# Kernel tuning notes

Hardware: AMD Instinct MI355X
Metric: run time of the kernel (lower is better)

Reference implementation:

```python
import jax, jax.numpy as jnp
import numpy as np
import math

# static configuration
SPATIAL_SHAPES = [(100, 150), (50, 75), (25, 38), (13, 19)]  # (H, W) per level
EMBED, HEADS, LEVELS, POINTS = 256, 8, 4, 4
HEAD_DIM = EMBED // HEADS
BS = 2
NV = sum(h * w for h, w in SPATIAL_SHAPES)  # 19947
NQ = NV  # encoder-style self-attention (value = query)


def _offset_bias():
    # replicate torch _init_weights grid init for sampling_offsets bias
    thetas = np.arange(HEADS, dtype=np.float32) * (2.0 * math.pi / HEADS)
    grid = np.stack([np.cos(thetas), np.sin(thetas)], -1)  # [H,2]
    grid = grid / np.abs(grid).max(-1, keepdims=True)
    grid = np.tile(grid[:, None, None, :], (1, LEVELS, POINTS, 1))
    for i in range(POINTS):
        grid[:, :, i, :] *= (i + 1)
    return jnp.asarray(grid.reshape(-1), dtype=jnp.float32)


def setup_inputs() -> dict:
    key = jax.random.key(0)
    ks = jax.random.split(key, 8)
    sc = 1.0 / math.sqrt(EMBED)
    return {
        "query": jax.random.normal(ks[0], (BS, NQ, EMBED), jnp.float32),
        "reference_points": jax.random.uniform(ks[1], (BS, NQ, LEVELS, 2), jnp.float32),
        "spatial_shapes": jnp.asarray(SPATIAL_SHAPES, dtype=jnp.int32),
        "W_off": jax.random.normal(ks[2], (EMBED, HEADS * LEVELS * POINTS * 2), jnp.float32) * 0.01,
        "b_off": _offset_bias(),
        "W_attn": jax.random.normal(ks[3], (EMBED, HEADS * LEVELS * POINTS), jnp.float32) * 0.01,
        "b_attn": jnp.zeros((HEADS * LEVELS * POINTS,), jnp.float32),
        "W_val": jax.random.normal(ks[4], (EMBED, EMBED), jnp.float32) * sc,
        "b_val": jnp.zeros((EMBED,), jnp.float32),
        "W_out": jax.random.normal(ks[5], (EMBED, EMBED), jnp.float32) * sc,
        "b_out": jnp.zeros((EMBED,), jnp.float32),
    }


def _bilinear_sample(value_l, loc_l, H, W):
    # value_l: [bs, H*W, heads, hd]; loc_l: [bs, nq, heads, P, 2] normalized coords
    # grid_sample semantics: align_corners=False, padding_mode='zeros'
    x = loc_l[..., 0] * W - 0.5
    y = loc_l[..., 1] * H - 0.5
    x0 = jnp.floor(x)
    y0 = jnp.floor(y)
    dx = x - x0
    dy = y - y0
    x0i = x0.astype(jnp.int32)
    y0i = y0.astype(jnp.int32)

    def gather(xi, yi):
        valid = (xi >= 0) & (xi < W) & (yi >= 0) & (yi < H)  # [bs,nq,h,P]
        idx = jnp.clip(yi, 0, H - 1) * W + jnp.clip(xi, 0, W - 1)
        bs, nq, h, P = idx.shape
        idx2 = idx.transpose(0, 1, 3, 2).reshape(bs, nq * P, h)[..., None]
        v = jnp.take_along_axis(value_l, idx2, axis=1)  # [bs, nq*P, h, hd]
        v = v.reshape(bs, nq, P, h, -1).transpose(0, 1, 3, 2, 4)  # [bs,nq,h,P,hd]
        return v * valid[..., None]

    w00 = ((1 - dx) * (1 - dy))[..., None]
    w01 = (dx * (1 - dy))[..., None]
    w10 = ((1 - dx) * dy)[..., None]
    w11 = (dx * dy)[..., None]
    return (gather(x0i, y0i) * w00 + gather(x0i + 1, y0i) * w01
            + gather(x0i, y0i + 1) * w10 + gather(x0i + 1, y0i + 1) * w11)


def reference(query, reference_points, spatial_shapes, W_off, b_off, W_attn, b_attn,
              W_val, b_val, W_out, b_out):
    bs, nq, _ = query.shape
    # value = query (encoder self-attn), identity = query
    value = (query @ W_val + b_val).reshape(bs, NV, HEADS, HEAD_DIM)
    offs = (query @ W_off + b_off).reshape(bs, nq, HEADS, LEVELS, POINTS, 2)
    attw = jax.nn.softmax((query @ W_attn + b_attn).reshape(bs, nq, HEADS, LEVELS * POINTS), axis=-1)
    attw = attw.reshape(bs, nq, HEADS, LEVELS, POINTS)
    # offset normalizer: (W, H) per level
    norm = jnp.stack([spatial_shapes[:, 1], spatial_shapes[:, 0]], -1).astype(query.dtype)
    loc = reference_points[:, :, None, :, None, :] + offs / norm[None, None, None, :, None, :]

    out = jnp.zeros((bs, nq, HEADS, HEAD_DIM), query.dtype)
    start = 0
    for lvl, (H, W) in enumerate(SPATIAL_SHAPES):
        value_l = value[:, start:start + H * W]  # static slice
        start += H * W
        sampled = _bilinear_sample(value_l, loc[:, :, :, lvl], H, W)  # [bs,nq,h,P,hd]
        out = out + jnp.einsum('bnhpc,bnhp->bnhc', sampled, attw[:, :, :, lvl, :])

    out = out.reshape(bs, nq, EMBED) @ W_out + b_out
    return out + query  # dropout(p=0) + identity
```

## Files before the change

### kernel.cpp

```cpp
#include <hip/hip_runtime.h>
#include <math.h>

#define HEADS     8
#define LEVELS    4
#define POINTS    4
#define HEAD_DIM  32
#define EMBED     256
#define NQ        19947
#define NV        19947
#define BS        2
#define M_ROWS    (BS * NQ)

typedef _Float16 h8 __attribute__((ext_vector_type(8)));
typedef _Float16 h4 __attribute__((ext_vector_type(4)));
typedef _Float16 h2 __attribute__((ext_vector_type(2)));
typedef float    f32x4 __attribute__((ext_vector_type(4)));
typedef unsigned short ushort8 __attribute__((ext_vector_type(8)));

static __device__ __forceinline__ int lvl_H(int l) {
    constexpr int v[4] = {100, 50, 25, 13}; return v[l];
}
static __device__ __forceinline__ int lvl_W(int l) {
    constexpr int v[4] = {150, 75, 38, 19}; return v[l];
}
static __device__ __forceinline__ int lvl_start(int l) {
    constexpr int v[4] = {0, 15000, 18750, 19700}; return v[l];
}

static __device__ __forceinline__ unsigned short f2h(float f) {
    _Float16 h = (_Float16)f;
    return __builtin_bit_cast(unsigned short, h);
}

static __device__ __forceinline__ void gload_lds16(const void* g, void* l) {
    __builtin_amdgcn_global_load_lds(
        (const __attribute__((address_space(1))) void*)g,
        (__attribute__((address_space(3))) void*)l, 16, 0, 0);
}

static __device__ __forceinline__ void pkacc_u(h2* acc, uint4 u, unsigned wbits) {
    const h2 wv = __builtin_bit_cast(h2, wbits);
    acc[0] = __builtin_bit_cast(h2, u.x) * wv + acc[0];
    acc[1] = __builtin_bit_cast(h2, u.y) * wv + acc[1];
    acc[2] = __builtin_bit_cast(h2, u.z) * wv + acc[2];
    acc[3] = __builtin_bit_cast(h2, u.w) * wv + acc[3];
}

__global__ __launch_bounds__(256) void pack_weights_kernel(
    const float* __restrict__ Wv, const float* __restrict__ Wo,
    const float* __restrict__ Wa, const float* __restrict__ Wout,
    unsigned short* __restrict__ Wcat, unsigned short* __restrict__ WoutT)
{
    const int tid = blockIdx.x * 256 + threadIdx.x;
    if (tid >= 896 * 32) return;
    const int row = tid >> 5;
    const int k8  = tid & 31;
    const float* src; int n_local, N; unsigned short* dstb; int r_local;
    if (row < 256)      { src = Wv;   n_local = row;       N = 256; dstb = Wcat;  r_local = row; }
    else if (row < 512) { src = Wo;   n_local = row - 256; N = 256; dstb = Wcat;  r_local = row; }
    else if (row < 640) { src = Wa;   n_local = row - 512; N = 128; dstb = Wcat;  r_local = row; }
    else                { src = Wout; n_local = row - 640; N = 256; dstb = WoutT; r_local = row - 640; }
    const int k = k8 * 8;
    ushort8 o;
    #pragma unroll
    for (int j = 0; j < 8; ++j)
        o[j] = f2h(src[(size_t)(k + j) * N + n_local]);
    const int g  = k8 >> 3;
    const int u2 = (k8 & 7) ^ (r_local & 7);
    *(ushort8*)((char*)dstb + (size_t)r_local * 512 + g * 128 + u2 * 16) = o;
}

template <int EPI>
__global__ __launch_bounds__(256) void mfma_gemm_kernel(
    const float* __restrict__ Aq,
    const unsigned short* __restrict__ Ah,
    const unsigned short* __restrict__ Bh,
    unsigned short* __restrict__ value_h,
    unsigned short* __restrict__ oa,
    const float* __restrict__ b_val, const float* __restrict__ b_off,
    const float* __restrict__ b_attn,
    const float* __restrict__ b_out,
    const float* __restrict__ qres,
    float* __restrict__ out)
{
    __shared__ alignas(16) char As[16384];
    __shared__ alignas(16) char Bs[16384];

    constexpr int NB = (EPI == 0) ? 5 : 2;
    const int id  = blockIdx.x;
    const int grp = id / (8 * NB);
    const int rem = id - grp * (8 * NB);
    const int bx  = grp * 8 + (rem & 7);
    const int by  = rem >> 3;

    const int t    = threadIdx.x;
    const int wid  = t >> 6;
    const int lane = t & 63;
    const int l15  = lane & 15;
    const int lhi  = lane >> 4;
    const int wr   = wid >> 1;
    const int wc   = wid & 1;
    const int m0   = bx * 128;
    const int n0   = by * 128;

    f32x4 acc[4][4] = {};

    auto stage = [&](int ks) {
        #pragma unroll
        for (int j = 0; j < 4; ++j) {
            const int q  = j * 256 + wid * 64 + lane;
            const int tr = q >> 3;
            const int u  = q & 7;
            int gr = m0 + tr; gr = gr < M_ROWS ? gr : (M_ROWS - 1);
            if (EPI == 0) {
                const float* src = Aq + (size_t)gr * 256 + ks * 64 + u * 8;
                const float4 v0 = *(const float4*)(src);
                const float4 v1 = *(const float4*)(src + 4);
                ushort8 o;
                o[0] = f2h(v0.x); o[1] = f2h(v0.y);
                o[2] = f2h(v0.z); o[3] = f2h(v0.w);
                o[4] = f2h(v1.x); o[5] = f2h(v1.y);
                o[6] = f2h(v1.z); o[7] = f2h(v1.w);
                *(ushort8*)&As[tr * 128 + (unsigned)(u ^ (tr & 7)) * 16] = o;
            } else {
                gload_lds16((const char*)Ah + (size_t)gr * 512 + ks * 128 + u * 16,
                            As + (j * 256 + wid * 64) * 16);
            }
            const int gn = n0 + tr;
            gload_lds16((const char*)Bh + (size_t)gn * 512 + ks * 128 + u * 16,
                        Bs + (j * 256 + wid * 64) * 16);
        }
    };

    stage(0);
    for (int ks = 0; ks < 4; ++ks) {
        __syncthreads();
        #pragma unroll
        for (int kc = 0; kc < 2; ++kc) {
            h8 a[4], b[4];
            #pragma unroll
            for (int i = 0; i < 4; ++i) {
                const int tr = wr * 64 + i * 16 + l15;
                const int ua = (kc * 4 + lhi) ^ (tr & 7);
                a[i] = *(const h8*)&As[tr * 128 + ua * 16];
                const int tn = wc * 64 + i * 16 + l15;
                const int ub = (kc * 4 + lhi) ^ (tn & 7);
                b[i] = *(const h8*)&Bs[tn * 128 + ub * 16];
            }
            #pragma unroll
            for (int i = 0; i < 4; ++i)
                #pragma unroll
                for (int j2 = 0; j2 < 4; ++j2)
                    acc[i][j2] = __builtin_amdgcn_mfma_f32_16x16x32_f16(
                        a[i], b[j2], acc[i][j2], 0, 0, 0);
        }
        if (ks < 3) { __syncthreads(); stage(ks + 1); }
    }

    if (EPI == 0) {
        if (by < 2) {
            #pragma unroll
            for (int j2 = 0; j2 < 4; ++j2) {
                const int gn = n0 + wc * 64 + j2 * 16 + l15;
                const float bias = b_val[gn];
                const int h = gn >> 5, ch = gn & 31;
                #pragma unroll
                for (int i = 0; i < 4; ++i) {
                    #pragma unroll
                    for (int r = 0; r < 4; ++r) {
                        const int gm = m0 + wr * 64 + i * 16 + lhi * 4 + r;
                        if (gm >= M_ROWS) continue;
                        const int bb  = gm >= NQ;
                        const int pix = gm - bb * NQ;
                        value_h[(((size_t)bb * 8 + h) * NV + pix) * 32 + ch] =
                            f2h(acc[i][j2][r] + bias);
                    }
                }
            }
        } else {
            #pragma unroll
            for (int j2 = 0; j2 < 4; ++j2) {
                const int gn  = n0 + wc * 64 + j2 * 16 + l15;
                const int col = gn - 256;
                const float bias = (col < 256) ? b_off[col] : b_attn[col - 256];
                #pragma unroll
                for (int i = 0; i < 4; ++i) {
                    #pragma unroll
                    for (int r = 0; r < 4; ++r) {
                        const int gm = m0 + wr * 64 + i * 16 + lhi * 4 + r;
                        if (gm >= M_ROWS) continue;
                        oa[(size_t)gm * 384 + col] = f2h(acc[i][j2][r] + bias);
                    }
                }
            }
        }
    } else {
        #pragma unroll
        for (int j2 = 0; j2 < 4; ++j2) {
            const int gn = n0 + wc * 64 + j2 * 16 + l15;
            const float bias = b_out[gn];
            #pragma unroll
            for (int i = 0; i < 4; ++i) {
                #pragma unroll
                for (int r = 0; r < 4; ++r) {
                    const int gm = m0 + wr * 64 + i * 16 + lhi * 4 + r;
                    if (gm >= M_ROWS) continue;
                    out[(size_t)gm * 256 + gn] =
                        acc[i][j2][r] + bias + qres[(size_t)gm * 256 + gn];
                }
            }
        }
    }
}

__global__ __launch_bounds__(256) void sample_kernel_v13(
    const unsigned short* __restrict__ value,
    const _Float16* __restrict__ oa,
    const float* __restrict__ refp,
    unsigned short* __restrict__ outa_h)
{
    __shared__ uint4 sw_lds[16][34];

    const int bx    = blockIdx.x;
    const int h     = bx & 7;
    const int chunk = bx >> 3;
    const int g     = threadIdx.x >> 3;
    const int l8    = threadIdx.x & 7;
    const int row   = chunk * 32 + g;
    const bool valid = row < M_ROWS;

    if (valid && l8 < 4) {
        const int lvl = l8;
        const _Float16* oar = oa + (size_t)row * 384;
        const h8 oxy = *(const h8*)(oar + h * 32 + lvl * 8);
        const h4 lgh = *(const h4*)(oar + 256 + h * 16 + lvl * 4);
        const float lg0 = (float)lgh[0], lg1 = (float)lgh[1];
        const float lg2 = (float)lgh[2], lg3 = (float)lgh[3];

        float mx = fmaxf(fmaxf(lg0, lg1), fmaxf(lg2, lg3));
        mx = fmaxf(mx, __shfl_xor(mx, 1));
        mx = fmaxf(mx, __shfl_xor(mx, 2));
        const float e0 = expf(lg0 - mx);
        const float e1 = expf(lg1 - mx);
        const float e2 = expf(lg2 - mx);
        const float e3 = expf(lg3 - mx);
        float sum = e0 + e1 + e2 + e3;
        sum += __shfl_xor(sum, 1);
        sum += __shfl_xor(sum, 2);
        const float inv = 1.f / sum;

        const float2 rr = *(const float2*)(refp + (size_t)row * 8 + lvl * 2);
        const int W = lvl_W(lvl), H = lvl_H(lvl), st = lvl_start(lvl);
        const float rx = rr.x * (float)W - 0.5f;
        const float ry = rr.y * (float)H - 0.5f;

        const float sxv[4] = {(float)oxy[0] + rx, (float)oxy[2] + rx,
                              (float)oxy[4] + rx, (float)oxy[6] + rx};
        const float syv[4] = {(float)oxy[1] + ry, (float)oxy[3] + ry,
                              (float)oxy[5] + ry, (float)oxy[7] + ry};
        const float ev[4]  = {e0 * inv, e1 * inv, e2 * inv, e3 * inv};

        #pragma unroll
        for (int p = 0; p < 4; ++p) {
            const float cx = sxv[p], cy = syv[p], wz = ev[p];
            const float fx = floorf(cx), fy = floorf(cy);
            const int x0 = (int)fx, y0 = (int)fy;
            const float dx = cx - fx, dy = cy - fy;
            const float omx = 1.f - dx, omy = 1.f - dy;
            float w00 = omx * omy * wz;
            float w01 = dx  * omy * wz;
            float w10 = omx * dy  * wz;
            float w11 = dx  * dy  * wz;
            const bool vx0 = (unsigned)x0       < (unsigned)W;
            const bool vx1 = (unsigned)(x0 + 1) < (unsigned)W;
            const bool vy0 = (unsigned)y0       < (unsigned)H;
            const bool vy1 = (unsigned)(y0 + 1) < (unsigned)H;
            w00 = (vx0 & vy0) ? w00 : 0.f;
            w01 = (vx1 & vy0) ? w01 : 0.f;
            w10 = (vx0 & vy1) ? w10 : 0.f;
            w11 = (vx1 & vy1) ? w11 : 0.f;
            const int px  = min(max(x0, 0), W - 2);
            const int xs0 = min(max(x0, 0), W - 1);
            const int xs1 = min(max(x0 + 1, 0), W - 1);
            const float wlo0 = (xs0 == px ? w00 : 0.f) + (xs1 == px ? w01 : 0.f);
            const float whi0 = (xs0 == px + 1 ? w00 : 0.f) + (xs1 == px + 1 ? w01 : 0.f);
            const float wlo1 = (xs0 == px ? w10 : 0.f) + (xs1 == px ? w11 : 0.f);
            const float whi1 = (xs0 == px + 1 ? w10 : 0.f) + (xs1 == px + 1 ? w11 : 0.f);
            const int ys0 = min(max(y0, 0), H - 1);
            const int ys1 = min(max(y0 + 1, 0), H - 1);
            const unsigned pix0 = (unsigned)(st + ys0 * W + px);
            const unsigned pix1 = (unsigned)(st + ys1 * W + px);
            uint4 e;
            e.x = pix0 | (pix1 << 16);
            e.y = ((unsigned)f2h(whi0) << 16) | (unsigned)f2h(wlo0);
            e.z = ((unsigned)f2h(whi1) << 16) | (unsigned)f2h(wlo1);
            e.w = 0;
            sw_lds[lvl * 4 + p][g] = e;
        }
    }
    __syncthreads();
    if (!valid) return;

    const int b = row >= NQ;
    const char* vb = (const char*)value + (((size_t)b * 8 + h) * NV) * 64 + l8 * 16;
    const unsigned selw = 0x01000100u + (unsigned)(l8 >> 2) * 0x02020202u;

    h2 acc[4] = {};
    #pragma unroll
    for (int s = 0; s < 16; ++s) {
        const uint4 e = sw_lds[s][g];
        const uint4 u0 = *(const uint4*)(vb + ((size_t)(e.x & 0xffffu) << 6));
        const uint4 u1 = *(const uint4*)(vb + ((size_t)(e.x >> 16)     << 6));
        const unsigned w0 = __builtin_amdgcn_perm(e.y, e.y, selw);
        const unsigned w1 = __builtin_amdgcn_perm(e.z, e.z, selw);
        pkacc_u(acc, u0, w0);
        pkacc_u(acc, u1, w1);
    }

    #pragma unroll
    for (int i = 0; i < 4; ++i) {
        const unsigned a = __builtin_bit_cast(unsigned, acc[i]);
        const unsigned o = (unsigned)__shfl_xor((int)a, 4);
        acc[i] = acc[i] + __builtin_bit_cast(h2, o);
    }

    if (l8 < 4) {
        const int bytecol = h * 64 + l8 * 16;
        const int g2 = bytecol >> 7;
        const int u2 = ((bytecol >> 4) & 7) ^ (row & 7);
        uint4 d;
        d.x = __builtin_bit_cast(unsigned, acc[0]);
        d.y = __builtin_bit_cast(unsigned, acc[1]);
        d.z = __builtin_bit_cast(unsigned, acc[2]);
        d.w = __builtin_bit_cast(unsigned, acc[3]);
        *(uint4*)((char*)outa_h + (size_t)row * 512 + g2 * 128 + u2 * 16) = d;
    }
}

extern "C" void kernel_launch(void* const* d_in, const int* in_sizes, int n_in,
                              void* d_out, int out_size, void* d_ws, size_t ws_size,
                              hipStream_t stream)
{
    const float* query  = (const float*)d_in[0];
    const float* refp   = (const float*)d_in[1];
    const float* W_off  = (const float*)d_in[3];
    const float* b_off  = (const float*)d_in[4];
    const float* W_attn = (const float*)d_in[5];
    const float* b_attn = (const float*)d_in[6];
    const float* W_val  = (const float*)d_in[7];
    const float* b_val  = (const float*)d_in[8];
    const float* W_out  = (const float*)d_in[9];
    const float* b_out  = (const float*)d_in[10];
    float* out = (float*)d_out;

    char* p = (char*)d_ws;
    unsigned short* oabf    = (unsigned short*)p;  p += (size_t)M_ROWS * 512;
    unsigned short* value_h = (unsigned short*)p;  p += (size_t)M_ROWS * 512;
    unsigned short* Wcat    = (unsigned short*)p;  p += (size_t)640 * 512;
    unsigned short* WoutT   = (unsigned short*)p;  p += (size_t)256 * 512;
    unsigned short* oa      = (unsigned short*)p;  p += (size_t)M_ROWS * 384 * 2;

    const dim3 blk(256);

    pack_weights_kernel<<<(896 * 32 + 255) / 256, blk, 0, stream>>>(
        W_val, W_off, W_attn, W_out, Wcat, WoutT);

    mfma_gemm_kernel<0><<<dim3(1560), blk, 0, stream>>>(
        query, nullptr, Wcat, value_h, oa, b_val, b_off, b_attn,
        nullptr, nullptr, nullptr);

    const int chunks = (M_ROWS + 31) / 32;
    sample_kernel_v13<<<chunks * 8, blk, 0, stream>>>(
        value_h, (const _Float16*)oa, refp, oabf);

    mfma_gemm_kernel<1><<<dim3(624), blk, 0, stream>>>(
        nullptr, oabf, WoutT, nullptr, nullptr, nullptr, nullptr, nullptr,
        b_out, query, out);
}
```

Measured before the change: 151.8 us.

## Halve GEMM row tile to 64 and remap waves across columns

Changes the MFMA GEMM block tile from 128x128 to 64x128, with each of four waves computing a 64x32 slab instead of a 2x2 wave grid. This doubles the number of blocks for both GEMMs and halves accumulator registers per thread, aiming at better occupancy and load balance across CUs. In exchange, each B tile is reused over fewer rows, so weight traffic rises.

```diff
diff --git a/kernel.cpp b/kernel.cpp
--- a/kernel.cpp
+++ b/kernel.cpp
@@ -10,6 +10,7 @@
 #define NV        19947
 #define BS        2
 #define M_ROWS    (BS * NQ)
+#define MT        624
 
 typedef _Float16 h8 __attribute__((ext_vector_type(8)));
 typedef _Float16 h4 __attribute__((ext_vector_type(4)));
@@ -83,7 +84,7 @@
     const float* __restrict__ qres,
     float* __restrict__ out)
 {
-    __shared__ alignas(16) char As[16384];
+    __shared__ alignas(16) char As[8192];
     __shared__ alignas(16) char Bs[16384];
 
     constexpr int NB = (EPI == 0) ? 5 : 2;
@@ -98,17 +99,15 @@
     const int lane = t & 63;
     const int l15  = lane & 15;
     const int lhi  = lane >> 4;
-    const int wr   = wid >> 1;
-    const int wc   = wid & 1;
-    const int m0   = bx * 128;
+    const int m0   = bx * 64;
     const int n0   = by * 128;
 
-    f32x4 acc[4][4] = {};
+    f32x4 acc[4][2] = {};
 
     auto stage = [&](int ks) {
         #pragma unroll
-        for (int j = 0; j < 4; ++j) {
-            const int q  = j * 256 + wid * 64 + lane;
+        for (int j = 0; j < 2; ++j) {
+            const int q  = j * 256 + t;
             const int tr = q >> 3;
             const int u  = q & 7;
             int gr = m0 + tr; gr = gr < M_ROWS ? gr : (M_ROWS - 1);
@@ -126,6 +125,12 @@
                 gload_lds16((const char*)Ah + (size_t)gr * 512 + ks * 128 + u * 16,
                             As + (j * 256 + wid * 64) * 16);
             }
+        }
+        #pragma unroll
+        for (int j = 0; j < 4; ++j) {
+            const int q  = j * 256 + t;
+            const int tr = q >> 3;
+            const int u  = q & 7;
             const int gn = n0 + tr;
             gload_lds16((const char*)Bh + (size_t)gn * 512 + ks * 128 + u * 16,
                         Bs + (j * 256 + wid * 64) * 16);
@@ -137,20 +142,23 @@
         __syncthreads();
         #pragma unroll
         for (int kc = 0; kc < 2; ++kc) {
-            h8 a[4], b[4];
+            h8 a[4], b[2];
             #pragma unroll
             for (int i = 0; i < 4; ++i) {
-                const int tr = wr * 64 + i * 16 + l15;
+                const int tr = i * 16 + l15;
                 const int ua = (kc * 4 + lhi) ^ (tr & 7);
                 a[i] = *(const h8*)&As[tr * 128 + ua * 16];
-                const int tn = wc * 64 + i * 16 + l15;
+            }
+            #pragma unroll
+            for (int j2 = 0; j2 < 2; ++j2) {
+                const int tn = wid * 32 + j2 * 16 + l15;
                 const int ub = (kc * 4 + lhi) ^ (tn & 7);
-                b[i] = *(const h8*)&Bs[tn * 128 + ub * 16];
+                b[j2] = *(const h8*)&Bs[tn * 128 + ub * 16];
             }
             #pragma unroll
             for (int i = 0; i < 4; ++i)
                 #pragma unroll
-                for (int j2 = 0; j2 < 4; ++j2)
+                for (int j2 = 0; j2 < 2; ++j2)
                     acc[i][j2] = __builtin_amdgcn_mfma_f32_16x16x32_f16(
                         a[i], b[j2], acc[i][j2], 0, 0, 0);
         }
@@ -160,15 +168,15 @@
     if (EPI == 0) {
         if (by < 2) {
             #pragma unroll
-            for (int j2 = 0; j2 < 4; ++j2) {
-                const int gn = n0 + wc * 64 + j2 * 16 + l15;
+            for (int j2 = 0; j2 < 2; ++j2) {
+                const int gn = n0 + wid * 32 + j2 * 16 + l15;
                 const float bias = b_val[gn];
                 const int h = gn >> 5, ch = gn & 31;
                 #pragma unroll
                 for (int i = 0; i < 4; ++i) {
                     #pragma unroll
                     for (int r = 0; r < 4; ++r) {
-                        const int gm = m0 + wr * 64 + i * 16 + lhi * 4 + r;
+                        const int gm = m0 + i * 16 + lhi * 4 + r;
                         if (gm >= M_ROWS) continue;
                         const int bb  = gm >= NQ;
                         const int pix = gm - bb * NQ;
@@ -179,15 +187,15 @@
             }
         } else {
             #pragma unroll
-            for (int j2 = 0; j2 < 4; ++j2) {
-                const int gn  = n0 + wc * 64 + j2 * 16 + l15;
+            for (int j2 = 0; j2 < 2; ++j2) {
+                const int gn  = n0 + wid * 32 + j2 * 16 + l15;
                 const int col = gn - 256;
                 const float bias = (col < 256) ? b_off[col] : b_attn[col - 256];
                 #pragma unroll
                 for (int i = 0; i < 4; ++i) {
                     #pragma unroll
                     for (int r = 0; r < 4; ++r) {
-                        const int gm = m0 + wr * 64 + i * 16 + lhi * 4 + r;
+                        const int gm = m0 + i * 16 + lhi * 4 + r;
                         if (gm >= M_ROWS) continue;
                         oa[(size_t)gm * 384 + col] = f2h(acc[i][j2][r] + bias);
                     }
@@ -196,14 +204,14 @@
         }
     } else {
         #pragma unroll
-        for (int j2 = 0; j2 < 4; ++j2) {
-            const int gn = n0 + wc * 64 + j2 * 16 + l15;
+        for (int j2 = 0; j2 < 2; ++j2) {
+            const int gn = n0 + wid * 32 + j2 * 16 + l15;
             const float bias = b_out[gn];
             #pragma unroll
             for (int i = 0; i < 4; ++i) {
                 #pragma unroll
                 for (int r = 0; r < 4; ++r) {
-                    const int gm = m0 + wr * 64 + i * 16 + lhi * 4 + r;
+                    const int gm = m0 + i * 16 + lhi * 4 + r;
                     if (gm >= M_ROWS) continue;
                     out[(size_t)gm * 256 + gn] =
                         acc[i][j2][r] + bias + qres[(size_t)gm * 256 + gn];
@@ -365,7 +373,7 @@
     pack_weights_kernel<<<(896 * 32 + 255) / 256, blk, 0, stream>>>(
         W_val, W_off, W_attn, W_out, Wcat, WoutT);
 
-    mfma_gemm_kernel<0><<<dim3(1560), blk, 0, stream>>>(
+    mfma_gemm_kernel<0><<<dim3(MT * 5), blk, 0, stream>>>(
         query, nullptr, Wcat, value_h, oa, b_val, b_off, b_attn,
         nullptr, nullptr, nullptr);
 
@@ -373,7 +381,7 @@
     sample_kernel_v13<<<chunks * 8, blk, 0, stream>>>(
         value_h, (const _Float16*)oa, refp, oabf);
 
-    mfma_gemm_kernel<1><<<dim3(624), blk, 0, stream>>>(
+    mfma_gemm_kernel<1><<<dim3(MT * 2), blk, 0, stream>>>(
         nullptr, oabf, WoutT, nullptr, nullptr, nullptr, nullptr, nullptr,
         b_out, query, out);
 }
```

New measurement: 137.7 us (median of 2 runs). -9.3%, faster.
